# Performance work log

Hardware: AMD Instinct MI355X
Metric: run time of the kernel (lower is better)

## Reference

```python
import jax, jax.numpy as jnp
import numpy as np

B, H, L, C = 16, 512, 4096, 1
LAM = 0.001  # kernel squash threshold (lam in LongConvKernel)


def setup_inputs() -> dict:
    key = jax.random.key(0)
    ks = jax.random.split(key, 5)
    u = jax.random.normal(ks[0], (B, H, L), jnp.float32)
    # LongConvKernel 'double_exp' init: K ~ N(0, 0.02^2) * exp(-(j/L) * (H//2)^(i/H))
    K = jax.random.normal(ks[1], (C, H, L), jnp.float32) * 0.02
    i = jnp.arange(H, dtype=jnp.float32)[:, None]
    j = jnp.arange(L, dtype=jnp.float32)[None, :]
    double_exp = jnp.exp(-(j / L) * jnp.power(float(H // 2), i / H))  # (H, L)
    kernel = K * double_exp[None]
    D = jax.random.normal(ks[2], (C, H), jnp.float32)  # skip connection params
    # TransposedLinear(C*H -> H): weight (d_output, d_input), kaiming-ish scale
    Wout = jax.random.normal(ks[3], (H, C * H), jnp.float32) / np.sqrt(C * H)
    bout = jax.random.normal(ks[4], (H,), jnp.float32) * 0.01
    return {"u": u, "kernel": kernel, "D": D, "Wout": Wout, "bout": bout}


def reference(u, kernel, D, Wout, bout):
    Lseq = u.shape[-1]
    # kernel squashing: relu(|k| - lam) * sign(k)  (soft-threshold)
    k = jax.nn.relu(jnp.abs(kernel) - LAM) * jnp.sign(kernel)  # (C, H, L)
    n = 2 * Lseq
    k_f = jnp.fft.rfft(k, n=n, axis=-1)            # (C, H, n//2+1) complex
    u_f = jnp.fft.rfft(u, n=n, axis=-1)            # (B, H, n//2+1) complex
    y_f = jnp.einsum('bhl,chl->bchl', u_f, k_f)    # pointwise multiply in freq
    y = jnp.fft.irfft(y_f, n=n, axis=-1)[..., :Lseq]  # (B, C, H, L)
    y = y + jnp.einsum('bhl,ch->bchl', u, D)       # skip term
    y = y.reshape(y.shape[0], C * H, Lseq)         # (B, C*H, L)
    y = jax.nn.gelu(y, approximate=False)          # activation (torch GELU = exact)
    # output_linear: TransposedLinear + swish postact
    y = jnp.einsum('bul,vu->bvl', y, Wout) + bout[None, :, None]
    y = jax.nn.silu(y)
    return y
```

## Files before the change

### kernel.cpp

```cpp
#include <hip/hip_runtime.h>
#include <hip/hip_bf16.h>
#include <math.h>

#define BB 16
#define HH 512
#define LL 4096
#define NFFT 8192
#define LAM 0.001f

typedef __attribute__((ext_vector_type(8))) short short8;
typedef __attribute__((ext_vector_type(4))) float floatx4;

#define R2C 0.70710678118654752f

__device__ __forceinline__ void cmul(float ar, float ai, float br, float bi,
                                     float& cr, float& ci) {
  cr = ar * br - ai * bi;
  ci = ar * bi + ai * br;
}

constexpr float W16C[8] = {1.f, 0.92387953f, 0.70710678f, 0.38268343f, 0.f,
                           -0.38268343f, -0.70710678f, -0.92387953f};
constexpr float W16S[8] = {0.f, -0.38268343f, -0.70710678f, -0.92387953f, -1.f,
                           -0.92387953f, -0.70710678f, -0.38268343f};
constexpr int BR8[8] = {0, 4, 2, 6, 1, 5, 3, 7};
constexpr float W16CB[8] = {W16C[0], W16C[4], W16C[2], W16C[6],
                            W16C[1], W16C[5], W16C[3], W16C[7]};
constexpr float W16SB[8] = {W16S[0], W16S[4], W16S[2], W16S[6],
                            W16S[1], W16S[5], W16S[3], W16S[7]};

__device__ __forceinline__ int slotf(int a) { return a ^ ((a >> 4) & 15); }

__device__ __forceinline__ void fft8(float* r, float* i) {
  float t0r = r[0] + r[4], t0i = i[0] + i[4], u0r = r[0] - r[4], u0i = i[0] - i[4];
  float t1r = r[1] + r[5], t1i = i[1] + i[5], u1r = r[1] - r[5], u1i = i[1] - i[5];
  float t2r = r[2] + r[6], t2i = i[2] + i[6], u2r = r[2] - r[6], u2i = i[2] - i[6];
  float t3r = r[3] + r[7], t3i = i[3] + i[7], u3r = r[3] - r[7], u3i = i[3] - i[7];
  float w1r = R2C * (u1r + u1i), w1i = R2C * (u1i - u1r);
  float w2r = u2i, w2i = -u2r;
  float w3r = R2C * (u3i - u3r), w3i = -R2C * (u3r + u3i);
  float p0r = t0r + t2r, p0i = t0i + t2i, q0r = t0r - t2r, q0i = t0i - t2i;
  float p1r = t1r + t3r, p1i = t1i + t3i, q1r = t1r - t3r, q1i = t1i - t3i;
  float s1r = q1i, s1i = -q1r;
  float v0r = u0r + w2r, v0i = u0i + w2i, x0r = u0r - w2r, x0i = u0i - w2i;
  float v1r = w1r + w3r, v1i = w1i + w3i, x1r = w1r - w3r, x1i = w1i - w3i;
  float y1r = x1i, y1i = -x1r;
  r[0] = p0r + p1r; i[0] = p0i + p1i;
  r[1] = p0r - p1r; i[1] = p0i - p1i;
  r[2] = q0r + s1r; i[2] = q0i + s1i;
  r[3] = q0r - s1r; i[3] = q0i - s1i;
  r[4] = v0r + v1r; i[4] = v0i + v1i;
  r[5] = v0r - v1r; i[5] = v0i - v1i;
  r[6] = x0r + y1r; i[6] = x0i + y1i;
  r[7] = x0r - y1r; i[7] = x0i - y1i;
}

__device__ __forceinline__ void fft8_pad4(float* r, float* i) {
  float x0r = r[0], x0i = i[0], x1r = r[1], x1i = i[1];
  float x2r = r[2], x2i = i[2], x3r = r[3], x3i = i[3];
  float w1r = R2C * (x1r + x1i), w1i = R2C * (x1i - x1r);
  float w2r = x2i, w2i = -x2r;
  float w3r = R2C * (x3i - x3r), w3i = -R2C * (x3r + x3i);
  float p0r = x0r + x2r, p0i = x0i + x2i, q0r = x0r - x2r, q0i = x0i - x2i;
  float p1r = x1r + x3r, p1i = x1i + x3i, q1r = x1r - x3r, q1i = x1i - x3i;
  float s1r = q1i, s1i = -q1r;
  float v0r = x0r + w2r, v0i = x0i + w2i, m0r = x0r - w2r, m0i = x0i - w2i;
  float v1r = w1r + w3r, v1i = w1i + w3i, m1r = w1r - w3r, m1i = w1i - w3i;
  float y1r = m1i, y1i = -m1r;
  r[0] = p0r + p1r; i[0] = p0i + p1i;
  r[1] = p0r - p1r; i[1] = p0i - p1i;
  r[2] = q0r + s1r; i[2] = q0i + s1i;
  r[3] = q0r - s1r; i[3] = q0i - s1i;
  r[4] = v0r + v1r; i[4] = v0i + v1i;
  r[5] = v0r - v1r; i[5] = v0i - v1i;
  r[6] = m0r + y1r; i[6] = m0i + y1i;
  r[7] = m0r - y1r; i[7] = m0i - y1i;
}

__device__ __forceinline__ void ifft8(float* r, float* i) {
  float p0r = r[0] + r[1], p0i = i[0] + i[1];
  float p1r = r[0] - r[1], p1i = i[0] - i[1];
  float q0r = r[2] + r[3], q0i = i[2] + i[3];
  float s1r = r[2] - r[3], s1i = i[2] - i[3];
  float v0r = r[4] + r[5], v0i = i[4] + i[5];
  float v1r = r[4] - r[5], v1i = i[4] - i[5];
  float x0r = r[6] + r[7], x0i = i[6] + i[7];
  float y1r = r[6] - r[7], y1i = i[6] - i[7];
  float q1r = -s1i, q1i = s1r;
  float x1r = -y1i, x1i = y1r;
  float t0r = p0r + q0r, t0i = p0i + q0i, t2r = p0r - q0r, t2i = p0i - q0i;
  float t1r = p1r + q1r, t1i = p1i + q1i, t3r = p1r - q1r, t3i = p1i - q1i;
  float a0r = v0r + x0r, a0i = v0i + x0i, a2r = v0r - x0r, a2i = v0i - x0i;
  float a1r = v1r + x1r, a1i = v1i + x1i, a3r = v1r - x1r, a3i = v1i - x1i;
  float u1r = R2C * (a1r - a1i), u1i = R2C * (a1r + a1i);
  float u2r = -a2i, u2i = a2r;
  float u3r = -R2C * (a3r + a3i), u3i = R2C * (a3r - a3i);
  r[0] = t0r + a0r; i[0] = t0i + a0i;  r[4] = t0r - a0r; i[4] = t0i - a0i;
  r[1] = t1r + u1r; i[1] = t1i + u1i;  r[5] = t1r - u1r; i[5] = t1i - u1i;
  r[2] = t2r + u2r; i[2] = t2i + u2i;  r[6] = t2r - u2r; i[6] = t2i - u2i;
  r[3] = t3r + u3r; i[3] = t3i + u3i;  r[7] = t3r - u3r; i[7] = t3i - u3i;
}

__device__ __forceinline__ void ifft8_head4(float* r, float* i) {
  float p0r = r[0] + r[1], p0i = i[0] + i[1];
  float p1r = r[0] - r[1], p1i = i[0] - i[1];
  float q0r = r[2] + r[3], q0i = i[2] + i[3];
  float s1r = r[2] - r[3], s1i = i[2] - i[3];
  float v0r = r[4] + r[5], v0i = i[4] + i[5];
  float v1r = r[4] - r[5], v1i = i[4] - i[5];
  float x0r = r[6] + r[7], x0i = i[6] + i[7];
  float y1r = r[6] - r[7], y1i = i[6] - i[7];
  float q1r = -s1i, q1i = s1r;
  float x1r = -y1i, x1i = y1r;
  float t0r = p0r + q0r, t0i = p0i + q0i, t2r = p0r - q0r, t2i = p0i - q0i;
  float t1r = p1r + q1r, t1i = p1i + q1i, t3r = p1r - q1r, t3i = p1i - q1i;
  float a0r = v0r + x0r, a0i = v0i + x0i, a2r = v0r - x0r, a2i = v0i - x0i;
  float a1r = v1r + x1r, a1i = v1i + x1i, a3r = v1r - x1r, a3i = v1i - x1i;
  float u1r = R2C * (a1r - a1i), u1i = R2C * (a1r + a1i);
  float u2r = -a2i, u2i = a2r;
  float u3r = -R2C * (a3r + a3i), u3i = R2C * (a3r - a3i);
  r[0] = t0r + a0r; i[0] = t0i + a0i;
  r[1] = t1r + u1r; i[1] = t1i + u1i;
  r[2] = t2r + u2r; i[2] = t2i + u2i;
  r[3] = t3r + u3r; i[3] = t3i + u3i;
}

__device__ __forceinline__ float gelu_exact(float y) {
  return 0.5f * y * (1.f + erff(y * 0.70710678118654752f));
}

template <int LOGJ>
__device__ __forceinline__ void r8_fwd(float2* sb, int t, const float4* tw) {
  const int J = 1 << LOGJ;
  const int j = t & (J - 1);
  const int base = (t >> LOGJ) << (LOGJ + 3);
  float xr[8], xi[8];
#pragma unroll
  for (int s = 0; s < 8; ++s) {
    float2 v = sb[slotf(base + j + (s << LOGJ))];
    xr[s] = v.x; xi[s] = v.y;
  }
  fft8(xr, xi);
#pragma unroll
  for (int q = 0; q < 4; ++q) {
    float4 w = tw[(q << LOGJ) + j];
    float tr, ti;
    cmul(xr[2 * q], xi[2 * q], w.x, w.y, tr, ti);
    sb[slotf(base + (BR8[2 * q] << LOGJ) + j)] = make_float2(tr, ti);
    cmul(xr[2 * q + 1], xi[2 * q + 1], w.z, w.w, tr, ti);
    sb[slotf(base + (BR8[2 * q + 1] << LOGJ) + j)] = make_float2(tr, ti);
  }
}

template <int LOGJ>
__device__ __forceinline__ void r8_inv(float2* sb, int t, const float4* tw) {
  const int J = 1 << LOGJ;
  const int j = t & (J - 1);
  const int base = (t >> LOGJ) << (LOGJ + 3);
  float xr[8], xi[8];
#pragma unroll
  for (int q = 0; q < 4; ++q) {
    float4 w = tw[(q << LOGJ) + j];
    float2 v0 = sb[slotf(base + (BR8[2 * q] << LOGJ) + j)];
    cmul(v0.x, v0.y, w.x, -w.y, xr[2 * q], xi[2 * q]);
    float2 v1 = sb[slotf(base + (BR8[2 * q + 1] << LOGJ) + j)];
    cmul(v1.x, v1.y, w.z, -w.w, xr[2 * q + 1], xi[2 * q + 1]);
  }
  ifft8(xr, xi);
#pragma unroll
  for (int s = 0; s < 8; ++s)
    sb[slotf(base + j + (s << LOGJ))] = make_float2(xr[s], xi[s]);
}

__device__ __forceinline__ void p1_scatter(float2* sb, int j, const float4* tw1,
                                           float* xr, float* xi) {
#pragma unroll
  for (int q = 0; q < 4; ++q) {
    float4 w = tw1[(q << 10) + j];
    float tr, ti;
    cmul(xr[2 * q], xi[2 * q], w.x, w.y, tr, ti);
    sb[slotf((BR8[2 * q] << 10) + j)] = make_float2(tr, ti);
    cmul(xr[2 * q + 1], xi[2 * q + 1], w.z, w.w, tr, ti);
    sb[slotf((BR8[2 * q + 1] << 10) + j)] = make_float2(tr, ti);
  }
}

__device__ __forceinline__ void p4_bins(float2* sb, int t, float* br_, float* bi_) {
  const int p = t >> 1, par = t & 1;
  const int a0 = (p << 4) + par;
  float xr[8], xi[8];
#pragma unroll
  for (int e = 0; e < 8; ++e) {
    float2 v = sb[slotf(a0 + 2 * e)];
    xr[e] = v.x; xi[e] = v.y;
  }
  fft8(xr, xi);
#pragma unroll
  for (int s = 0; s < 8; ++s) {
    float tr, ti;
    if (par) { cmul(xr[s], xi[s], W16CB[s], W16SB[s], tr, ti); }
    else { tr = xr[s]; ti = xi[s]; }
    float orr = __shfl_xor(tr, 1);
    float oii = __shfl_xor(ti, 1);
    br_[s] = par ? (orr - tr) : (tr + orr);
    bi_[s] = par ? (oii - ti) : (ti + oii);
  }
}

__device__ __forceinline__ void p4_inv(float2* sb, int t, float* br_, float* bi_) {
  const int p = t >> 1, par = t & 1;
  const int a0 = (p << 4) + par;
  float yr[8], yi[8];
#pragma unroll
  for (int s = 0; s < 8; ++s) {
    float orr = __shfl_xor(br_[s], 1);
    float oii = __shfl_xor(bi_[s], 1);
    float er = par ? (orr - br_[s]) : (br_[s] + orr);
    float ei = par ? (oii - bi_[s]) : (bi_[s] + oii);
    if (par) { float tr, ti; cmul(er, ei, W16CB[s], -W16SB[s], tr, ti); er = tr; ei = ti; }
    yr[s] = er; yi[s] = ei;
  }
  ifft8(yr, yi);
#pragma unroll
  for (int e = 0; e < 8; ++e)
    sb[slotf(a0 + 2 * e)] = make_float2(yr[e], yi[e]);
}

__global__ __launch_bounds__(1024) void twgen_kernel(float4* __restrict__ tw1,
                                                     float4* __restrict__ tw2,
                                                     float4* __restrict__ tw3) {
  const int j = threadIdx.x;
#pragma unroll
  for (int q = 0; q < 4; ++q) {
    const int m0 = BR8[2 * q], m1 = BR8[2 * q + 1];
    float s0, c0, s1, c1;
    const float a1 = -6.283185307179586f / 8192.f;
    sincosf(a1 * (float)(j * m0), &s0, &c0);
    sincosf(a1 * (float)(j * m1), &s1, &c1);
    tw1[(q << 10) + j] = make_float4(c0, s0, c1, s1);
    if (j < 128) {
      const float a2 = -6.283185307179586f / 1024.f;
      sincosf(a2 * (float)(j * m0), &s0, &c0);
      sincosf(a2 * (float)(j * m1), &s1, &c1);
      tw2[(q << 7) + j] = make_float4(c0, s0, c1, s1);
    }
    if (j < 16) {
      const float a3 = -6.283185307179586f / 128.f;
      sincosf(a3 * (float)(j * m0), &s0, &c0);
      sincosf(a3 * (float)(j * m1), &s1, &c1);
      tw3[(q << 4) + j] = make_float4(c0, s0, c1, s1);
    }
  }
}

__global__ void wconv_kernel(const float* __restrict__ W,
                             __hip_bfloat16* __restrict__ Wb) {
  int i = blockIdx.x * 256 + threadIdx.x;
  Wb[i] = __float2bfloat16(W[i]);
}

__global__ __launch_bounds__(1024)
void kf_kernel(const float* __restrict__ kern, const float* __restrict__ D,
               float* __restrict__ Kf, const float4* __restrict__ tw1,
               const float4* __restrict__ tw2, const float4* __restrict__ tw3) {
  __shared__ __align__(16) float2 sb[NFFT];
  __shared__ __align__(16) float4 ltw2[512];
  __shared__ __align__(16) float4 ltw3[64];
  const int t = threadIdx.x;
  const int h = blockIdx.x;
  const float* kr = kern + (size_t)h * LL;
  if (t < 512) ltw2[t] = tw2[t];
  if (t < 64) ltw3[t] = tw3[t];
  {
    float xr[8], xi[8];
#pragma unroll
    for (int s = 0; s < 4; ++s) {
      float kv = kr[t + (s << 10)];
      float a = fabsf(kv) - LAM;
      float sq = (a > 0.f) ? ((kv > 0.f) ? a : -a) : 0.f;
      xr[s] = sq * (1.f / 8192.f);
      xi[s] = 0.f;
    }
    fft8_pad4(xr, xi);
    p1_scatter(sb, t, tw1, xr, xi);
  }
  __syncthreads();
  r8_fwd<7>(sb, t, ltw2);
  __syncthreads();
  r8_fwd<4>(sb, t, ltw3);
  {
    float br_[8], bi_[8];
    p4_bins(sb, t, br_, bi_);
    const float dsc = D[h] * (1.f / 8192.f);
    float4* out4 = (float4*)(Kf + (size_t)h * NFFT * 2) + (t << 2);
#pragma unroll
    for (int q = 0; q < 4; ++q)
      out4[q] = make_float4(br_[2 * q] + dsc, bi_[2 * q],
                            br_[2 * q + 1] + dsc, bi_[2 * q + 1]);
  }
}

__global__ __launch_bounds__(1024)
void fftconv_kernel(const float* __restrict__ u, const float* __restrict__ Kf,
                    __hip_bfloat16* __restrict__ g, const float4* __restrict__ tw1,
                    const float4* __restrict__ tw2, const float4* __restrict__ tw3) {
  __shared__ __align__(16) float2 sb[NFFT];
  __shared__ __align__(16) float4 ltw2[512];
  __shared__ __align__(16) float4 ltw3[64];
  const int t = threadIdx.x;
  const int h = blockIdx.x;
  const int p = blockIdx.y;
  const int b0 = 2 * p, b1 = 2 * p + 1;
  const float* u0 = u + ((size_t)(b0 * HH + h)) * LL;
  const float* u1 = u + ((size_t)(b1 * HH + h)) * LL;

  if (t < 512) ltw2[t] = tw2[t];
  if (t < 64) ltw3[t] = tw3[t];

  {
    float xr[8], xi[8];
#pragma unroll
    for (int s = 0; s < 4; ++s) {
      xr[s] = u0[t + (s << 10)];
      xi[s] = u1[t + (s << 10)];
    }
    fft8_pad4(xr, xi);
    p1_scatter(sb, t, tw1, xr, xi);
  }
  __syncthreads();
  r8_fwd<7>(sb, t, ltw2);
  __syncthreads();
  r8_fwd<4>(sb, t, ltw3);
  {
    float br_[8], bi_[8];
    p4_bins(sb, t, br_, bi_);
    const float4* kf4 = (const float4*)(Kf + (size_t)h * NFFT * 2) + (t << 2);
#pragma unroll
    for (int q = 0; q < 4; ++q) {
      float4 kk = kf4[q];
      float tr, ti;
      cmul(br_[2 * q], bi_[2 * q], kk.x, kk.y, tr, ti);
      br_[2 * q] = tr; bi_[2 * q] = ti;
      cmul(br_[2 * q + 1], bi_[2 * q + 1], kk.z, kk.w, tr, ti);
      br_[2 * q + 1] = tr; bi_[2 * q + 1] = ti;
    }
    p4_inv(sb, t, br_, bi_);
  }
  r8_inv<4>(sb, t, ltw3);
  __syncthreads();
  r8_inv<7>(sb, t, ltw2);
  __syncthreads();
  {
    float xr[8], xi[8];
#pragma unroll
    for (int q = 0; q < 4; ++q) {
      float4 w = tw1[(q << 10) + t];
      float2 v0 = sb[slotf((BR8[2 * q] << 10) + t)];
      cmul(v0.x, v0.y, w.x, -w.y, xr[2 * q], xi[2 * q]);
      float2 v1 = sb[slotf((BR8[2 * q + 1] << 10) + t)];
      cmul(v1.x, v1.y, w.z, -w.w, xr[2 * q + 1], xi[2 * q + 1]);
    }
    ifft8_head4(xr, xi);
    __hip_bfloat16* g0 = g + ((size_t)(b0 * HH + h)) * LL;
    __hip_bfloat16* g1 = g + ((size_t)(b1 * HH + h)) * LL;
#pragma unroll
    for (int s = 0; s < 4; ++s) {
      g0[t + (s << 10)] = __float2bfloat16(gelu_exact(xr[s]));
      g1[t + (s << 10)] = __float2bfloat16(gelu_exact(xi[s]));
    }
  }
}

__global__ __launch_bounds__(256, 4) void gemm_kernel(
    const __hip_bfloat16* __restrict__ Wb, const __hip_bfloat16* __restrict__ g,
    const float* __restrict__ bout, float* __restrict__ out) {
  __shared__ unsigned short At[2][128][40];
  __shared__ unsigned short Bt[2][4096];
  const int id = blockIdx.x;
  const int w = (id & 7) * 256 + (id >> 3);
  const int vt = w & 3;
  const int lt = (w >> 2) & 31;
  const int b = w >> 7;
  const int tid = threadIdx.x;
  const int wave = tid >> 6;
  const int ln = tid & 63;
  const int wr = wave >> 1, wc = wave & 1;
  const int lane16 = ln & 15;
  const int quad = ln >> 4;
  const int lbase0 = lt * 128;

  const int a_m = tid >> 2;
  const int a_c = (tid & 3) * 8;
  const int b_h = tid >> 4;
  const int b_l = (tid & 15) * 8;

  const unsigned short* Ag = (const unsigned short*)Wb + (size_t)(vt * 128) * HH;
  const unsigned short* gb = (const unsigned short*)g + (size_t)b * HH * LL + lbase0;

  floatx4 acc[4][4];
#pragma unroll
  for (int mi = 0; mi < 4; ++mi)
#pragma unroll
    for (int ni = 0; ni < 4; ++ni) acc[mi][ni] = (floatx4){0.f, 0.f, 0.f, 0.f};

  int4 la0, la1, lb0, lb1;
#define GLOAD(K0)                                                         \
  la0 = *(const int4*)(Ag + (size_t)a_m * HH + (K0) + a_c);               \
  la1 = *(const int4*)(Ag + (size_t)(a_m + 64) * HH + (K0) + a_c);        \
  lb0 = *(const int4*)(gb + (size_t)((K0) + b_h) * LL + b_l);             \
  lb1 = *(const int4*)(gb + (size_t)((K0) + b_h + 16) * LL + b_l);
#define LWRITE(BUF)                                                       \
  *(int4*)&At[BUF][a_m][a_c] = la0;                                       \
  *(int4*)&At[BUF][a_m + 64][a_c] = la1;                                  \
  {                                                                       \
    unsigned short vs[8];                                                 \
    *(int4*)vs = lb0;                                                     \
    _Pragma("unroll") for (int e = 0; e < 8; ++e) {                       \
      const int l = b_l + e;                                              \
      const int blk = (l * 4 + (b_h >> 3)) ^ ((l >> 3) & 7);              \
      Bt[BUF][blk * 8 + (b_h & 7)] = vs[e];                               \
    }                                                                     \
    *(int4*)vs = lb1;                                                     \
    _Pragma("unroll") for (int e = 0; e < 8; ++e) {                       \
      const int l = b_l + e;                                              \
      const int h2 = b_h + 16;                                            \
      const int blk = (l * 4 + (h2 >> 3)) ^ ((l >> 3) & 7);               \
      Bt[BUF][blk * 8 + (h2 & 7)] = vs[e];                                \
    }                                                                     \
  }

  GLOAD(0);
  LWRITE(0);
  __syncthreads();

  const int kk = quad * 8;
  for (int s = 0; s < 16; ++s) {
    const int cur = s & 1;
    if (s < 15) { GLOAD((s + 1) * 32); }
    short8 af[4], bf[4];
#pragma unroll
    for (int mi = 0; mi < 4; ++mi)
      af[mi] = *(const short8*)&At[cur][wr * 64 + mi * 16 + lane16][kk];
#pragma unroll
    for (int ni = 0; ni < 4; ++ni) {
      const int nloc = wc * 64 + ni * 16 + lane16;
      const int blk = (nloc * 4 + quad) ^ ((nloc >> 3) & 7);
      bf[ni] = *(const short8*)&Bt[cur][blk * 8];
    }
#pragma unroll
    for (int mi = 0; mi < 4; ++mi)
#pragma unroll
      for (int ni = 0; ni < 4; ++ni)
        acc[mi][ni] = __builtin_amdgcn_mfma_f32_16x16x32_bf16(af[mi], bf[ni],
                                                              acc[mi][ni], 0, 0, 0);
    if (s < 15) { LWRITE(cur ^ 1); }
    __syncthreads();
  }

#pragma unroll
  for (int mi = 0; mi < 4; ++mi) {
#pragma unroll
    for (int r = 0; r < 4; ++r) {
      const int m = vt * 128 + wr * 64 + mi * 16 + quad * 4 + r;
      const float bias = bout[m];
#pragma unroll
      for (int ni = 0; ni < 4; ++ni) {
        const int n = lbase0 + wc * 64 + ni * 16 + lane16;
        float y = acc[mi][ni][r] + bias;
        y = y / (1.f + __expf(-y));
        out[((size_t)(b * HH + m)) * LL + n] = y;
      }
    }
  }
#undef GLOAD
#undef LWRITE
}

extern "C" void kernel_launch(void* const* d_in, const int* in_sizes, int n_in,
                              void* d_out, int out_size, void* d_ws, size_t ws_size,
                              hipStream_t stream) {
  const float* u = (const float*)d_in[0];
  const float* kern = (const float*)d_in[1];
  const float* D = (const float*)d_in[2];
  const float* Wout = (const float*)d_in[3];
  const float* bout = (const float*)d_in[4];
  float* out = (float*)d_out;

  char* ws = (char*)d_ws;
  const size_t KF_BYTES = (size_t)HH * NFFT * sizeof(float2);
  const size_t G_BYTES = (size_t)BB * HH * LL * 2;
  float* Kf = (float*)ws;
  __hip_bfloat16* g = (__hip_bfloat16*)(ws + KF_BYTES);
  __hip_bfloat16* Wb = (__hip_bfloat16*)(ws + KF_BYTES + 2 * G_BYTES);
  float4* tw1 = (float4*)(ws + KF_BYTES + G_BYTES);
  float4* tw2 = tw1 + 4 * 1024;
  float4* tw3 = tw2 + 4 * 128;

  twgen_kernel<<<dim3(1), dim3(1024), 0, stream>>>(tw1, tw2, tw3);
  wconv_kernel<<<dim3((HH * HH) / 256), dim3(256), 0, stream>>>(Wout, Wb);
  kf_kernel<<<dim3(HH), dim3(1024), 0, stream>>>(kern, D, Kf, tw1, tw2, tw3);
  fftconv_kernel<<<dim3(HH, BB / 2), dim3(1024), 0, stream>>>(u, Kf, g, tw1, tw2, tw3);
  gemm_kernel<<<dim3(2048), dim3(256), 0, stream>>>(Wb, g, bout, out);
}
```

Measured before the change: 477.9 us.

## Use 512-thread GEMM blocks with 2x4 wave grid and deeper global prefetch

Doubles the GEMM block to 8 waves, arranged 2x4, so each wave computes a 64x32 sub-tile and each thread loads half as much per k-step. Global loads are issued two stages ahead, right after the LDS write, instead of at the top of the iteration, and the final redundant barrier is dropped. The goal is more waves to hide latency and lower per-thread register pressure. The cost is fewer MFMAs per LDS fragment read, so LDS reuse per wave drops.

```diff
diff --git a/kernel.cpp b/kernel.cpp
--- a/kernel.cpp
+++ b/kernel.cpp
@@ -371,7 +371,7 @@
   }
 }
 
-__global__ __launch_bounds__(256, 4) void gemm_kernel(
+__global__ __launch_bounds__(512) void gemm_kernel(
     const __hip_bfloat16* __restrict__ Wb, const __hip_bfloat16* __restrict__ g,
     const float* __restrict__ bout, float* __restrict__ out) {
   __shared__ unsigned short At[2][128][40];
@@ -384,7 +384,8 @@
   const int tid = threadIdx.x;
   const int wave = tid >> 6;
   const int ln = tid & 63;
-  const int wr = wave >> 1, wc = wave & 1;
+  const int wr = wave >> 2;
+  const int wc = wave & 3;
   const int lane16 = ln & 15;
   const int quad = ln >> 4;
   const int lbase0 = lt * 128;
@@ -397,64 +398,57 @@
   const unsigned short* Ag = (const unsigned short*)Wb + (size_t)(vt * 128) * HH;
   const unsigned short* gb = (const unsigned short*)g + (size_t)b * HH * LL + lbase0;
 
-  floatx4 acc[4][4];
+  floatx4 acc[4][2];
 #pragma unroll
   for (int mi = 0; mi < 4; ++mi)
 #pragma unroll
-    for (int ni = 0; ni < 4; ++ni) acc[mi][ni] = (floatx4){0.f, 0.f, 0.f, 0.f};
-
-  int4 la0, la1, lb0, lb1;
+    for (int ni = 0; ni < 2; ++ni) acc[mi][ni] = (floatx4){0.f, 0.f, 0.f, 0.f};
+
+  int4 la, lb;
 #define GLOAD(K0)                                                         \
-  la0 = *(const int4*)(Ag + (size_t)a_m * HH + (K0) + a_c);               \
-  la1 = *(const int4*)(Ag + (size_t)(a_m + 64) * HH + (K0) + a_c);        \
-  lb0 = *(const int4*)(gb + (size_t)((K0) + b_h) * LL + b_l);             \
-  lb1 = *(const int4*)(gb + (size_t)((K0) + b_h + 16) * LL + b_l);
+  la = *(const int4*)(Ag + (size_t)a_m * HH + (K0) + a_c);                \
+  lb = *(const int4*)(gb + (size_t)((K0) + b_h) * LL + b_l);
 #define LWRITE(BUF)                                                       \
-  *(int4*)&At[BUF][a_m][a_c] = la0;                                       \
-  *(int4*)&At[BUF][a_m + 64][a_c] = la1;                                  \
+  *(int4*)&At[BUF][a_m][a_c] = la;                                        \
   {                                                                       \
     unsigned short vs[8];                                                 \
-    *(int4*)vs = lb0;                                                     \
+    *(int4*)vs = lb;                                                      \
     _Pragma("unroll") for (int e = 0; e < 8; ++e) {                       \
       const int l = b_l + e;                                              \
       const int blk = (l * 4 + (b_h >> 3)) ^ ((l >> 3) & 7);              \
       Bt[BUF][blk * 8 + (b_h & 7)] = vs[e];                               \
     }                                                                     \
-    *(int4*)vs = lb1;                                                     \
-    _Pragma("unroll") for (int e = 0; e < 8; ++e) {                       \
-      const int l = b_l + e;                                              \
-      const int h2 = b_h + 16;                                            \
-      const int blk = (l * 4 + (h2 >> 3)) ^ ((l >> 3) & 7);               \
-      Bt[BUF][blk * 8 + (h2 & 7)] = vs[e];                                \
-    }                                                                     \
   }
 
   GLOAD(0);
   LWRITE(0);
+  GLOAD(32);
   __syncthreads();
 
   const int kk = quad * 8;
   for (int s = 0; s < 16; ++s) {
     const int cur = s & 1;
-    if (s < 15) { GLOAD((s + 1) * 32); }
-    short8 af[4], bf[4];
+    short8 af[4], bf[2];
 #pragma unroll
     for (int mi = 0; mi < 4; ++mi)
       af[mi] = *(const short8*)&At[cur][wr * 64 + mi * 16 + lane16][kk];
 #pragma unroll
-    for (int ni = 0; ni < 4; ++ni) {
-      const int nloc = wc * 64 + ni * 16 + lane16;
+    for (int ni = 0; ni < 2; ++ni) {
+      const int nloc = wc * 32 + ni * 16 + lane16;
       const int blk = (nloc * 4 + quad) ^ ((nloc >> 3) & 7);
       bf[ni] = *(const short8*)&Bt[cur][blk * 8];
     }
 #pragma unroll
     for (int mi = 0; mi < 4; ++mi)
 #pragma unroll
-      for (int ni = 0; ni < 4; ++ni)
+      for (int ni = 0; ni < 2; ++ni)
         acc[mi][ni] = __builtin_amdgcn_mfma_f32_16x16x32_bf16(af[mi], bf[ni],
                                                               acc[mi][ni], 0, 0, 0);
-    if (s < 15) { LWRITE(cur ^ 1); }
-    __syncthreads();
+    if (s < 15) {
+      LWRITE(cur ^ 1);
+      if (s < 14) GLOAD((s + 2) * 32);
+      __syncthreads();
+    }
   }
 
 #pragma unroll
@@ -464,8 +458,8 @@
       const int m = vt * 128 + wr * 64 + mi * 16 + quad * 4 + r;
       const float bias = bout[m];
 #pragma unroll
-      for (int ni = 0; ni < 4; ++ni) {
-        const int n = lbase0 + wc * 64 + ni * 16 + lane16;
+      for (int ni = 0; ni < 2; ++ni) {
+        const int n = lbase0 + wc * 32 + ni * 16 + lane16;
         float y = acc[mi][ni][r] + bias;
         y = y / (1.f + __expf(-y));
         out[((size_t)(b * HH + m)) * LL + n] = y;
@@ -500,5 +494,5 @@
   wconv_kernel<<<dim3((HH * HH) / 256), dim3(256), 0, stream>>>(Wout, Wb);
   kf_kernel<<<dim3(HH), dim3(1024), 0, stream>>>(kern, D, Kf, tw1, tw2, tw3);
   fftconv_kernel<<<dim3(HH, BB / 2), dim3(1024), 0, stream>>>(u, Kf, g, tw1, tw2, tw3);
-  gemm_kernel<<<dim3(2048), dim3(256), 0, stream>>>(Wb, g, bout, out);
-}
+  gemm_kernel<<<dim3(2048), dim3(512), 0, stream>>>(Wb, g, bout, out);
+}
```

Result: no change. 479.7 us (+0.4%).
